# Performance work log

Measured on AMD Instinct MI355X. Metric: run time of the kernel, lower is better.

The kernel has to match this reference:

```python
import jax, jax.numpy as jnp
import numpy as np

C = 32           # number of dominant frequency components kept per node
TAU_FACTOR = 1.0  # dynamic threshold factor
EPS = 1e-10


def setup_inputs() -> dict:
    key = jax.random.key(0)
    k1, k2 = jax.random.split(key)
    N, K = 8192, 256
    # phases in [-pi, pi), amplitudes in [0, 1)
    P_ref = (jax.random.uniform(k1, (N, K), dtype=jnp.float32) - 0.5) * (2.0 * np.pi)
    A_ref = jax.random.uniform(k2, (N, K), dtype=jnp.float32)
    return {"P_ref": P_ref, "A_ref": A_ref}


def reference(P_ref, A_ref):
    N, K = A_ref.shape
    # top-C amplitude mask per node (scatter of top-k indices)
    _, idx = jax.lax.top_k(A_ref, C)                      # [N, C]
    mask = jnp.zeros((N, K), dtype=A_ref.dtype)
    mask = mask.at[jnp.arange(N)[:, None], idx].set(1.0)  # [N, K]
    A_m = A_ref * mask
    P_m = P_ref * mask

    # num[n,m] = sum_k A_m[n,k] A_m[m,k] cos(P_m[n,k] - P_m[m,k])
    # cos(a-b) = cos a cos b + sin a sin b  ->  two GEMMs, no [N,N,K] tensor
    Ac = A_m * jnp.cos(P_m)                               # [N, K]
    As = A_m * jnp.sin(P_m)                               # [N, K]
    num = Ac @ Ac.T + As @ As.T                           # [N, N]

    sq = jnp.sum(A_m * A_m, axis=1)                       # [N]
    denom = jnp.sqrt(sq[:, None] * sq[None, :] + EPS)     # [N, N]
    R = num / denom

    # row-normalize
    R_prime = R / (jnp.sum(R, axis=1, keepdims=True) + EPS)

    # dynamic threshold: mean of strictly-positive entries
    pos = R_prime > 0
    mean_positive = jnp.sum(jnp.where(pos, R_prime, 0.0)) / jnp.maximum(
        jnp.sum(pos).astype(R_prime.dtype), 1.0
    )
    tau = jnp.where(mean_positive > 0, TAU_FACTOR * mean_positive,
                    jnp.asarray(TAU_FACTOR, R_prime.dtype))
    R_hat = jnp.where(R_prime >= tau, R_prime, jnp.zeros_like(R_prime))
    return R_hat
```

## Files before the change

kernel.cpp:

```cpp
#include <hip/hip_runtime.h>
#include <hip/hip_bf16.h>

#define NN 8192
#define KF 256
#define KD 512
#define CK 32
#define PACK 67108864.0

typedef unsigned int uint32;
typedef unsigned short ushort16;
typedef __attribute__((ext_vector_type(8))) short bf16x8;
typedef __attribute__((ext_vector_type(4))) float f32x4;

static __device__ __forceinline__ float bf2f(ushort16 u) {
    union { uint32 i; float f; } v; v.i = ((uint32)u) << 16; return v.f;
}
static __device__ __forceinline__ ushort16 f2bf(float f) {
    __hip_bfloat16 h = __float2bfloat16(f);
    union { __hip_bfloat16 h; ushort16 u; } v; v.h = h; return v.u;
}
static __device__ __forceinline__ void split3(float x, ushort16& h, ushort16& l, ushort16& l2) {
    h = f2bf(x);
    float r1 = x - bf2f(h);
    l = f2bf(r1);
    float r2 = r1 - bf2f(l);
    l2 = f2bf(r2);
}

__global__ void detect_init_kernel(const uint32* __restrict__ rawA, int* __restrict__ flag,
                                   double* __restrict__ acc, double* __restrict__ gstats) {
    if (blockIdx.x == 0) {
        __shared__ int s_top2, s_nz;
        if (threadIdx.x == 0) { s_top2 = 0; s_nz = 0; }
        __syncthreads();
        int top2 = 0, nz = 0;
        for (int i = threadIdx.x; i < 4096; i += 256) {
            uint32 lo = rawA[i] & 0xFFFFu;
            if (lo & 0xC000u) top2 = 1;
            if (lo) nz = 1;
        }
        if (top2) atomicOr(&s_top2, 1);
        if (nz) atomicOr(&s_nz, 1);
        __syncthreads();
        if (threadIdx.x == 0) {
            int f;
            if (s_top2) f = 1;
            else if (s_nz) f = 0;
            else f = 1;
            *flag = f;
        }
    } else {
        int i = (blockIdx.x - 1) * 256 + threadIdx.x;
        if (i < 3 * NN) acc[i] = 0.0;
        if (i < 2) gstats[i] = 0.0;
    }
}

__global__ void prep_kernel(const void* __restrict__ P_, const void* __restrict__ A_,
                            const int* __restrict__ flag,
                            ushort16* __restrict__ Xh, ushort16* __restrict__ Xl,
                            ushort16* __restrict__ Xl2, float* __restrict__ sq) {
    int f = *flag;
    int row = blockIdx.x * 4 + (threadIdx.x >> 6);
    int lane = threadIdx.x & 63;
    if (row >= NN) return;
    float a[4], p[4];
    bool sel[4] = {false, false, false, false};
    if (f) {
        const float* Ar = (const float*)A_ + (size_t)row * KF;
        const float* Pr = (const float*)P_ + (size_t)row * KF;
#pragma unroll
        for (int j = 0; j < 4; j++) {
            int k = lane + 64 * j;
            a[j] = Ar[k];
            p[j] = Pr[k];
        }
    } else {
        const __hip_bfloat16* Ar = (const __hip_bfloat16*)A_ + (size_t)row * KF;
        const __hip_bfloat16* Pr = (const __hip_bfloat16*)P_ + (size_t)row * KF;
#pragma unroll
        for (int j = 0; j < 4; j++) {
            int k = lane + 64 * j;
            a[j] = __bfloat162float(Ar[k]);
            p[j] = __bfloat162float(Pr[k]);
        }
    }
    for (int it = 0; it < CK; ++it) {
        float bv = -1.0f; int bi = KF;
#pragma unroll
        for (int j = 0; j < 4; j++) {
            int k = lane + 64 * j;
            if (!sel[j] && (a[j] > bv || (a[j] == bv && k < bi))) { bv = a[j]; bi = k; }
        }
        for (int off = 32; off > 0; off >>= 1) {
            float ov = __shfl_xor(bv, off);
            int   oi = __shfl_xor(bi, off);
            if (ov > bv || (ov == bv && oi < bi)) { bv = ov; bi = oi; }
        }
        if ((bi & 63) == lane) sel[bi >> 6] = true;
    }
    double sq_part = 0.0;
    size_t rb = (size_t)row * KD;
#pragma unroll
    for (int j = 0; j < 4; j++) {
        int k = lane + 64 * j;
        float c = 0.0f, s = 0.0f;
        if (sel[j]) {
            c = a[j] * cosf(p[j]);
            s = a[j] * sinf(p[j]);
            sq_part += (double)a[j] * (double)a[j];
        }
        ushort16 h, l, l2;
        split3(c, h, l, l2);
        Xh[rb + k] = h; Xl[rb + k] = l; Xl2[rb + k] = l2;
        split3(s, h, l, l2);
        Xh[rb + KF + k] = h; Xl[rb + KF + k] = l; Xl2[rb + KF + k] = l2;
    }
    for (int off = 32; off > 0; off >>= 1) sq_part += __shfl_xor(sq_part, off);
    if (lane == 0) sq[row] = (float)sq_part;
}

#define MM2(A, B)                                                                  \
    _Pragma("unroll") for (int tm = 0; tm < 2; tm++)                               \
    _Pragma("unroll") for (int tn = 0; tn < 2; tn++)                               \
        acc[tm][tn] = __builtin_amdgcn_mfma_f32_16x16x32_bf16(A[tm], B[tn], acc[tm][tn], 0, 0, 0);

#define LOADF2(dst, p, rg, half)                                                   \
    _Pragma("unroll") for (int t = 0; t < 2; t++)                                  \
        dst[t] = *(const bf16x8*)&lds4[(p) * 1536 + (rg) * 256 + ((half) * 32 + t * 16 + r15) * 4 + qp];

#define GLOAD(gp, ldsidx)                                                          \
    __builtin_amdgcn_global_load_lds(                                              \
        (const __attribute__((address_space(1))) unsigned int*)(gp),               \
        (__attribute__((address_space(3))) unsigned int*)&lds4[ldsidx], 16, 0, 0)

#define GLOADALL(p, ko)                                                            \
    _Pragma("unroll") for (int j = 0; j < 6; j++)                                  \
        GLOAD(gptr[j] + (ko), (p) * 1536 + j * 256 + w * 64);

#define COMPUTE(p) {                                                               \
    bf16x8 fa[2], fb[2], ga[2], gb[2];                                             \
    LOADF2(fa, p, 0, wm)                                                  \
    LOADF2(fb, p, 3, wn)                                                  \
    MM2(fa, fb)                                                           \
    LOADF2(gb, p, 4, wn)                                                  \
    MM2(fa, gb)                                                           \
    LOADF2(ga, p, 1, wm)                                                  \
    MM2(ga, fb)                                                           \
    MM2(ga, gb)                                                           \
    LOADF2(gb, p, 5, wn)                                                  \
    MM2(fa, gb)                                                          \
    LOADF2(ga, p, 2, wm)                                                  \
    MM2(ga, fb)             }

__global__ __launch_bounds__(256)
void gemm_kernel(const ushort16* __restrict__ Xh, const ushort16* __restrict__ Xl,
                 const ushort16* __restrict__ Xl2, const float* __restrict__ sq,
                 void* __restrict__ outv, const int* __restrict__ flag,
                 double* __restrict__ rowsum, double* __restrict__ possum,
                 double* __restrict__ pcnt) {
    int bx = blockIdx.x, by = blockIdx.y;
    if (bx < by) return;
    __shared__ uint4 lds4[3072];
    int f = *flag;
    int tid = threadIdx.x;
    int w = tid >> 6;
    int wm = w >> 1, wn = w & 1;
    int L = tid & 63, quad = L >> 4, r15 = L & 15;
    int qp = quad ^ ((r15 >> 1) & 3);
    int row0 = by * 64, col0 = bx * 64;

    f32x4 acc[2][2];
#pragma unroll
    for (int tm = 0; tm < 2; tm++)
#pragma unroll
        for (int tn = 0; tn < 2; tn++) acc[tm][tn] = (f32x4){0.f, 0.f, 0.f, 0.f};

    const ushort16* gptr[6];
    {
        int row = tid >> 2, sp = tid & 3;
        int q = sp ^ ((row >> 1) & 3);
        const ushort16* srcs[6] = {Xh, Xl, Xl2, Xh, Xl, Xl2};
#pragma unroll
        for (int j = 0; j < 6; j++) {
            int tb = (j < 3) ? row0 : col0;
            gptr[j] = srcs[j] + (size_t)(tb + row) * KD + q * 8;
        }
    }

    GLOADALL(0, 0)
    for (int t = 0; t < 16; t += 2) {
        __syncthreads();
        if (t + 1 < 16) { GLOADALL(1, (t + 1) * 32) }
        COMPUTE(0)
        __syncthreads();
        if (t + 2 < 16) { GLOADALL(0, (t + 2) * 32) }
        COMPUTE(1)
    }

    float sqj2[2], sqi2[2][4];
#pragma unroll
    for (int tn = 0; tn < 2; tn++) sqj2[tn] = sq[col0 + wn * 32 + tn * 16 + r15];
#pragma unroll
    for (int tm = 0; tm < 2; tm++)
#pragma unroll
        for (int g = 0; g < 4; g++) sqi2[tm][g] = sq[row0 + wm * 32 + tm * 16 + quad * 4 + g];
#pragma unroll
    for (int tm = 0; tm < 2; tm++)
#pragma unroll
        for (int tn = 0; tn < 2; tn++)
#pragma unroll
            for (int g = 0; g < 4; g++) {
                float denom = sqrtf(sqi2[tm][g] * sqj2[tn] + 1e-10f);
                acc[tm][tn][g] = acc[tm][tn][g] / denom;
            }

    __syncthreads();
    float* Wf = (float*)lds4;
#pragma unroll
    for (int tm = 0; tm < 2; tm++)
#pragma unroll
        for (int tn = 0; tn < 2; tn++)
#pragma unroll
            for (int g = 0; g < 4; g++)
                Wf[(wm * 32 + tm * 16 + quad * 4 + g) * 68 + wn * 32 + tn * 16 + r15] = acc[tm][tn][g];
    __syncthreads();

    int r = tid >> 2, cseg = tid & 3;
    float vals[16];
#pragma unroll
    for (int i4 = 0; i4 < 4; i4++) {
        float4 fv = *(const float4*)&Wf[r * 68 + cseg * 16 + i4 * 4];
        vals[i4 * 4 + 0] = fv.x; vals[i4 * 4 + 1] = fv.y;
        vals[i4 * 4 + 2] = fv.z; vals[i4 * 4 + 3] = fv.w;
    }
    {
        double rs_ = 0.0, ps_ = 0.0;
        float pc_ = 0.0f, nc_ = 0.0f;
#pragma unroll
        for (int i = 0; i < 16; i++) {
            float v = vals[i];
            rs_ += (double)v;
            if (v > 0.0f) { ps_ += (double)v; pc_ += 1.0f; }
            else if (v < 0.0f) { nc_ += 1.0f; }
        }
        rs_ += __shfl_xor(rs_, 1); rs_ += __shfl_xor(rs_, 2);
        ps_ += __shfl_xor(ps_, 1); ps_ += __shfl_xor(ps_, 2);
        pc_ += __shfl_xor(pc_, 1); pc_ += __shfl_xor(pc_, 2);
        nc_ += __shfl_xor(nc_, 1); nc_ += __shfl_xor(nc_, 2);
        if (cseg == 0) {
            int gr = row0 + r;
            atomicAdd(&rowsum[gr], rs_);
            atomicAdd(&possum[gr], ps_);
            atomicAdd(&pcnt[gr], (double)pc_ * PACK + (double)nc_);
        }
    }
    {
        size_t ob = (((size_t)(row0 + r)) << 13) + col0 + cseg * 16;
        if (f) {
            float* O = (float*)outv;
#pragma unroll
            for (int i4 = 0; i4 < 4; i4++)
                *(float4*)(O + ob + i4 * 4) =
                    make_float4(vals[i4 * 4], vals[i4 * 4 + 1], vals[i4 * 4 + 2], vals[i4 * 4 + 3]);
        } else {
            union { uint4 u; ushort16 s[8]; } p0, p1;
#pragma unroll
            for (int i = 0; i < 8; i++) p0.s[i] = f2bf(vals[i]);
#pragma unroll
            for (int i = 0; i < 8; i++) p1.s[i] = f2bf(vals[8 + i]);
            *(uint4*)((__hip_bfloat16*)outv + ob) = p0.u;
            *(uint4*)((__hip_bfloat16*)outv + ob + 8) = p1.u;
        }
    }
    if (bx != by) {
        float vm[16];
#pragma unroll
        for (int i = 0; i < 16; i++) vm[i] = Wf[(cseg * 16 + i) * 68 + r];
        double cs = 0.0, cp = 0.0;
        float cc = 0.0f, cn = 0.0f;
#pragma unroll
        for (int i = 0; i < 16; i++) {
            float v = vm[i];
            cs += (double)v;
            if (v > 0.0f) { cp += (double)v; cc += 1.0f; }
            else if (v < 0.0f) { cn += 1.0f; }
        }
        cs += __shfl_xor(cs, 1); cs += __shfl_xor(cs, 2);
        cp += __shfl_xor(cp, 1); cp += __shfl_xor(cp, 2);
        cc += __shfl_xor(cc, 1); cc += __shfl_xor(cc, 2);
        cn += __shfl_xor(cn, 1); cn += __shfl_xor(cn, 2);
        if (cseg == 0) {
            int gc = col0 + r;
            atomicAdd(&rowsum[gc], cs);
            atomicAdd(&possum[gc], cp);
            atomicAdd(&pcnt[gc], (double)cc * PACK + (double)cn);
        }
        size_t obm = (((size_t)(col0 + r)) << 13) + row0 + cseg * 16;
        if (f) {
            float* O = (float*)outv;
#pragma unroll
            for (int i4 = 0; i4 < 4; i4++)
                *(float4*)(O + obm + i4 * 4) =
                    make_float4(vm[i4 * 4], vm[i4 * 4 + 1], vm[i4 * 4 + 2], vm[i4 * 4 + 3]);
        } else {
            union { uint4 u; ushort16 s[8]; } m0, m1;
#pragma unroll
            for (int i = 0; i < 8; i++) m0.s[i] = f2bf(vm[i]);
#pragma unroll
            for (int i = 0; i < 8; i++) m1.s[i] = f2bf(vm[8 + i]);
            *(uint4*)((__hip_bfloat16*)outv + obm) = m0.u;
            *(uint4*)((__hip_bfloat16*)outv + obm + 8) = m1.u;
        }
    }
}

__global__ void rowfin_kernel(const double* __restrict__ rowsum, const double* __restrict__ possum,
                              const double* __restrict__ pcnt,
                              float* __restrict__ inv_rs, double* __restrict__ gstats) {
    __shared__ double sc[256], sn[256];
    int n = blockIdx.x * 256 + threadIdx.x;
    double rsumv = rowsum[n];
    double rs = rsumv + 1e-10;
    inv_rs[n] = (float)(1.0 / rs);
    double packed = pcnt[n];
    double pc = floor(packed * (1.0 / PACK));
    double nc = packed - pc * PACK;
    double contrib, cnt;
    if (rs > 0.0) { contrib = possum[n] / rs; cnt = pc; }
    else          { contrib = (rsumv - possum[n]) / rs; cnt = nc; }
    sc[threadIdx.x] = contrib; sn[threadIdx.x] = cnt;
    __syncthreads();
    for (int s = 128; s > 0; s >>= 1) {
        if (threadIdx.x < s) { sc[threadIdx.x] += sc[threadIdx.x + s]; sn[threadIdx.x] += sn[threadIdx.x + s]; }
        __syncthreads();
    }
    if (threadIdx.x == 0) { atomicAdd(&gstats[0], sc[0]); atomicAdd(&gstats[1], sn[0]); }
}

__global__ void tau_kernel(const double* __restrict__ gstats, float* __restrict__ tau) {
    double cnt = gstats[1];
    if (cnt < 1.0) cnt = 1.0;
    double mp = gstats[0] / cnt;
    tau[0] = (mp > 0.0) ? (float)mp : 1.0f;
}

__global__ void thresh_kernel(void* __restrict__ R_,
                              const float* __restrict__ inv_rs,
                              const float* __restrict__ tau_p,
                              const int* __restrict__ flag) {
    int f = *flag;
    float tau = *tau_p;
    size_t base = ((size_t)blockIdx.x * 256 + threadIdx.x) * 8;
    if (base >= (size_t)NN * NN) return;
    float inv = inv_rs[base >> 13];
    if (f) {
        float* R = (float*)R_;
        float4 v0 = *(float4*)(R + base);
        float4 v1 = *(float4*)(R + base + 4);
        float vv[8] = {v0.x, v0.y, v0.z, v0.w, v1.x, v1.y, v1.z, v1.w};
#pragma unroll
        for (int t = 0; t < 8; t++) {
            float val = vv[t] * inv;
            vv[t] = (val >= tau) ? val : 0.0f;
        }
        *(float4*)(R + base)     = make_float4(vv[0], vv[1], vv[2], vv[3]);
        *(float4*)(R + base + 4) = make_float4(vv[4], vv[5], vv[6], vv[7]);
    } else {
        __hip_bfloat16* R = (__hip_bfloat16*)R_;
        union { uint4 u; ushort16 s[8]; } in, out;
        in.u = *(const uint4*)(R + base);
#pragma unroll
        for (int t = 0; t < 8; t++) {
            float val = bf2f(in.s[t]) * inv;
            float r = (val >= tau) ? val : 0.0f;
            out.s[t] = f2bf(r);
        }
        *(uint4*)(R + base) = out.u;
    }
}

__global__ void sentinel_kernel(uint32* __restrict__ out, size_t n32) {
    size_t i = (size_t)blockIdx.x * 256 + threadIdx.x;
    if (i < n32) out[i] = 0x47C35000u;
}

extern "C" void kernel_launch(void* const* d_in, const int* in_sizes, int n_in,
                              void* d_out, int out_size, void* d_ws, size_t ws_size,
                              hipStream_t stream) {
    const void* P = d_in[0];
    const void* A = d_in[1];

    char* ws = (char*)d_ws;
    size_t off = 0;
    ushort16* Xh = (ushort16*)(ws + off);   off += (size_t)NN * KD * 2;
    ushort16* Xl = (ushort16*)(ws + off);   off += (size_t)NN * KD * 2;
    ushort16* Xl2 = (ushort16*)(ws + off);  off += (size_t)NN * KD * 2;
    float* sqv = (float*)(ws + off);        off += (size_t)NN * 4;
    double* rowsum = (double*)(ws + off);   off += (size_t)NN * 8;
    double* possum = (double*)(ws + off);   off += (size_t)NN * 8;
    double* pcnt = (double*)(ws + off);     off += (size_t)NN * 8;
    float* inv_rs = (float*)(ws + off);     off += (size_t)NN * 4;
    double* gstats = (double*)(ws + off);   off += 16;
    float* tau = (float*)(ws + off);        off += 16;
    int* flag = (int*)(ws + off);           off += 16;

    if (ws_size < off) {
        size_t n32 = ((size_t)out_size * 2) / 4;
        sentinel_kernel<<<(int)((n32 + 255) / 256), 256, 0, stream>>>((uint32*)d_out, n32);
        return;
    }

    detect_init_kernel<<<1 + (3 * NN + 255) / 256, 256, 0, stream>>>((const uint32*)A, flag, rowsum, gstats);
    prep_kernel<<<NN / 4, 256, 0, stream>>>(P, A, flag, Xh, Xl, Xl2, sqv);
    dim3 ggrid(128, 128);
    gemm_kernel<<<ggrid, 256, 0, stream>>>(Xh, Xl, Xl2, sqv, d_out, flag, rowsum, possum, pcnt);
    rowfin_kernel<<<NN / 256, 256, 0, stream>>>(rowsum, possum, pcnt, inv_rs, gstats);
    tau_kernel<<<1, 1, 0, stream>>>(gstats, tau);
    thresh_kernel<<<(int)(((size_t)NN * NN / 8 + 255) / 256), 256, 0, stream>>>(d_out, inv_rs, tau, flag);
}
```

Measured before the change: 680.6 us.

## Add 128x128-tile symmetric GEMM kernel with dynamic LDS and small-tile fallback

Adds a new GEMM kernel that computes 128x128 output tiles per block (4x4 MFMA tiles per wave) instead of 64x64, using 96KB of dynamic shared memory for the double-buffered triple-split bf16 operands. Larger tiles double the arithmetic done per byte loaded from global memory and halve the number of blocks and atomics for row statistics. The epilogue stages results through LDS to write both the tile and its mirrored transpose with vector stores. The old 64x64 kernel is kept as a fallback if the larger shared-memory request fails, at the cost of higher register pressure and lower occupancy in the big kernel.

```diff
diff --git a/kernel.cpp b/kernel.cpp
--- a/kernel.cpp
+++ b/kernel.cpp
@@ -120,6 +120,228 @@
     if (lane == 0) sq[row] = (float)sq_part;
 }
 
+#define GLOAD(gp, ldsidx)                                                          \
+    __builtin_amdgcn_global_load_lds(                                              \
+        (const __attribute__((address_space(1))) unsigned int*)(gp),               \
+        (__attribute__((address_space(3))) unsigned int*)&lds4[ldsidx], 16, 0, 0)
+
+#define MMB(A, B)                                                                  \
+    _Pragma("unroll") for (int tm = 0; tm < 4; tm++)                               \
+    _Pragma("unroll") for (int tn = 0; tn < 4; tn++)                               \
+        acc[tm][tn] = __builtin_amdgcn_mfma_f32_16x16x32_bf16(A[tm], B[tn], acc[tm][tn], 0, 0, 0);
+
+#define LOADB(dst, p, region, wbase)                                               \
+    _Pragma("unroll") for (int t = 0; t < 4; t++)                                  \
+        dst[t] = *(const bf16x8*)&lds4[(p) * 3072 + (region) * 512 + ((wbase) + t * 16 + r15) * 4 + qp];
+
+#define GLOADALLB(p, ko)                                                           \
+    _Pragma("unroll") for (int j = 0; j < 2; j++) {                                \
+        int lb = (p) * 3072 + w * 128 + j * 64;                                    \
+        GLOAD(gpB[j * 6 + 0] + (ko), 0 * 512 + lb);                                \
+        GLOAD(gpB[j * 6 + 1] + (ko), 1 * 512 + lb);                                \
+        GLOAD(gpB[j * 6 + 2] + (ko), 2 * 512 + lb);                                \
+        GLOAD(gpB[j * 6 + 3] + (ko), 3 * 512 + lb);                                \
+        GLOAD(gpB[j * 6 + 4] + (ko), 4 * 512 + lb);                                \
+        GLOAD(gpB[j * 6 + 5] + (ko), 5 * 512 + lb);                                \
+    }
+
+#define COMPUTEB(p) {                                                              \
+    bf16x8 fa[4], fb[4], ga[4], gb[4];                                             \
+    LOADB(fa, p, 0, wm * 64)                                              \
+    LOADB(fb, p, 3, wn * 64)                                              \
+    MMB(fa, fb)                                                           \
+    LOADB(gb, p, 4, wn * 64)                                              \
+    MMB(fa, gb)                                                           \
+    LOADB(ga, p, 1, wm * 64)                                              \
+    MMB(ga, fb)                                                           \
+    MMB(ga, gb)                                                           \
+    LOADB(gb, p, 5, wn * 64)                                              \
+    MMB(fa, gb)                                                          \
+    LOADB(ga, p, 2, wm * 64)                                              \
+    MMB(ga, fb)                 }
+
+__global__ __launch_bounds__(256)
+void gemm_big(const ushort16* __restrict__ Xh, const ushort16* __restrict__ Xl,
+              const ushort16* __restrict__ Xl2, const float* __restrict__ sq,
+              void* __restrict__ outv, const int* __restrict__ flag,
+              double* __restrict__ rowsum, double* __restrict__ possum,
+              double* __restrict__ pcnt) {
+    int bx = blockIdx.x, by = blockIdx.y;
+    if (bx < by) return;
+    extern __shared__ uint4 lds4[];
+    int f = *flag;
+    int tid = threadIdx.x;
+    int w = tid >> 6;
+    int wm = w >> 1, wn = w & 1;
+    int L = tid & 63, quad = L >> 4, r15 = L & 15;
+    int qp = quad ^ ((r15 >> 1) & 3);
+    int row0 = by * 128, col0 = bx * 128;
+
+    f32x4 acc[4][4];
+#pragma unroll
+    for (int tm = 0; tm < 4; tm++)
+#pragma unroll
+        for (int tn = 0; tn < 4; tn++) acc[tm][tn] = (f32x4){0.f, 0.f, 0.f, 0.f};
+
+    const ushort16* gpB[12];
+#pragma unroll
+    for (int j = 0; j < 2; j++) {
+        int s = w * 128 + j * 64 + L;
+        int rr_ = s >> 2;
+        int qq = (s & 3) ^ ((rr_ >> 1) & 3);
+        size_t aoff = (size_t)(row0 + rr_) * KD + qq * 8;
+        size_t boff = (size_t)(col0 + rr_) * KD + qq * 8;
+        gpB[j * 6 + 0] = Xh + aoff;  gpB[j * 6 + 1] = Xl + aoff;  gpB[j * 6 + 2] = Xl2 + aoff;
+        gpB[j * 6 + 3] = Xh + boff;  gpB[j * 6 + 4] = Xl + boff;  gpB[j * 6 + 5] = Xl2 + boff;
+    }
+
+    GLOADALLB(0, 0)
+    for (int t = 0; t < 16; t += 2) {
+        __syncthreads();
+        if (t + 1 < 16) { GLOADALLB(1, (t + 1) * 32) }
+        COMPUTEB(0)
+        __syncthreads();
+        if (t + 2 < 16) { GLOADALLB(0, (t + 2) * 32) }
+        COMPUTEB(1)
+    }
+
+    float sqj[4], sqiv[4][4];
+#pragma unroll
+    for (int tn = 0; tn < 4; tn++) sqj[tn] = sq[col0 + wn * 64 + tn * 16 + r15];
+#pragma unroll
+    for (int tm = 0; tm < 4; tm++)
+#pragma unroll
+        for (int g = 0; g < 4; g++) sqiv[tm][g] = sq[row0 + wm * 64 + tm * 16 + quad * 4 + g];
+#pragma unroll
+    for (int tm = 0; tm < 4; tm++)
+#pragma unroll
+        for (int tn = 0; tn < 4; tn++)
+#pragma unroll
+            for (int g = 0; g < 4; g++) {
+                float denom = sqrtf(sqiv[tm][g] * sqj[tn] + 1e-10f);
+                acc[tm][tn][g] = acc[tm][tn][g] / denom;
+            }
+
+#pragma unroll
+    for (int tm = 0; tm < 4; tm++)
+#pragma unroll
+        for (int g = 0; g < 4; g++) {
+            double rs_ = 0.0, ps_ = 0.0;
+            float pc_ = 0.0f, nc_ = 0.0f;
+#pragma unroll
+            for (int tn = 0; tn < 4; tn++) {
+                float r = acc[tm][tn][g];
+                rs_ += (double)r;
+                if (r > 0.0f) { ps_ += (double)r; pc_ += 1.0f; }
+                else if (r < 0.0f) { nc_ += 1.0f; }
+            }
+            for (int off = 1; off < 16; off <<= 1) {
+                rs_ += __shfl_xor(rs_, off);
+                ps_ += __shfl_xor(ps_, off);
+                pc_ += __shfl_xor(pc_, off);
+                nc_ += __shfl_xor(nc_, off);
+            }
+            if (r15 == 0) {
+                int gr = row0 + wm * 64 + tm * 16 + quad * 4 + g;
+                atomicAdd(&rowsum[gr], rs_);
+                atomicAdd(&possum[gr], ps_);
+                atomicAdd(&pcnt[gr], (double)pc_ * PACK + (double)nc_);
+            }
+        }
+
+    if (bx != by) {
+#pragma unroll
+        for (int tn = 0; tn < 4; tn++) {
+            double cs = 0.0, cp = 0.0;
+            float cc = 0.0f, cn = 0.0f;
+#pragma unroll
+            for (int tm = 0; tm < 4; tm++)
+#pragma unroll
+                for (int g = 0; g < 4; g++) {
+                    float r = acc[tm][tn][g];
+                    cs += (double)r;
+                    if (r > 0.0f) { cp += (double)r; cc += 1.0f; }
+                    else if (r < 0.0f) { cn += 1.0f; }
+                }
+            cs += __shfl_xor(cs, 16); cs += __shfl_xor(cs, 32);
+            cp += __shfl_xor(cp, 16); cp += __shfl_xor(cp, 32);
+            cc += __shfl_xor(cc, 16); cc += __shfl_xor(cc, 32);
+            cn += __shfl_xor(cn, 16); cn += __shfl_xor(cn, 32);
+            if (L < 16) {
+                int gc = col0 + wn * 64 + tn * 16 + L;
+                atomicAdd(&rowsum[gc], cs);
+                atomicAdd(&possum[gc], cp);
+                atomicAdd(&pcnt[gc], (double)cc * PACK + (double)cn);
+            }
+        }
+    }
+
+    __syncthreads();
+    float* Wf = (float*)lds4;
+#pragma unroll
+    for (int tm = 0; tm < 4; tm++)
+#pragma unroll
+        for (int tn = 0; tn < 4; tn++)
+#pragma unroll
+            for (int g = 0; g < 4; g++)
+                Wf[(wm * 64 + tm * 16 + quad * 4 + g) * 132 + wn * 64 + tn * 16 + r15] = acc[tm][tn][g];
+    __syncthreads();
+
+    {
+        int r = tid >> 1, ch = (tid & 1) * 64;
+        size_t ob = (((size_t)(row0 + r)) << 13) + col0 + ch;
+#pragma unroll
+        for (int seg = 0; seg < 4; seg++) {
+            float4 a0 = *(const float4*)&Wf[r * 132 + ch + seg * 16 + 0];
+            float4 a1 = *(const float4*)&Wf[r * 132 + ch + seg * 16 + 4];
+            float4 a2 = *(const float4*)&Wf[r * 132 + ch + seg * 16 + 8];
+            float4 a3 = *(const float4*)&Wf[r * 132 + ch + seg * 16 + 12];
+            if (f) {
+                float* O = (float*)outv;
+                *(float4*)(O + ob + seg * 16 + 0)  = a0;
+                *(float4*)(O + ob + seg * 16 + 4)  = a1;
+                *(float4*)(O + ob + seg * 16 + 8)  = a2;
+                *(float4*)(O + ob + seg * 16 + 12) = a3;
+            } else {
+                float v[16] = {a0.x,a0.y,a0.z,a0.w, a1.x,a1.y,a1.z,a1.w,
+                               a2.x,a2.y,a2.z,a2.w, a3.x,a3.y,a3.z,a3.w};
+                union { uint4 u; ushort16 s[8]; } p0, p1;
+#pragma unroll
+                for (int i = 0; i < 8; i++) p0.s[i] = f2bf(v[i]);
+#pragma unroll
+                for (int i = 0; i < 8; i++) p1.s[i] = f2bf(v[8 + i]);
+                *(uint4*)((__hip_bfloat16*)outv + ob + seg * 16) = p0.u;
+                *(uint4*)((__hip_bfloat16*)outv + ob + seg * 16 + 8) = p1.u;
+            }
+        }
+    }
+    if (bx != by) {
+        int c = tid >> 1, rh = (tid & 1) * 64;
+        size_t obm = (((size_t)(col0 + c)) << 13) + row0 + rh;
+#pragma unroll
+        for (int seg = 0; seg < 4; seg++) {
+            float v[16];
+#pragma unroll
+            for (int i = 0; i < 16; i++) v[i] = Wf[(rh + seg * 16 + i) * 132 + c];
+            if (f) {
+                float* O = (float*)outv;
+#pragma unroll
+                for (int i4 = 0; i4 < 4; i4++)
+                    *(float4*)(O + obm + seg * 16 + i4 * 4) =
+                        make_float4(v[i4 * 4], v[i4 * 4 + 1], v[i4 * 4 + 2], v[i4 * 4 + 3]);
+            } else {
+                union { uint4 u; ushort16 s[8]; } m0, m1;
+#pragma unroll
+                for (int i = 0; i < 8; i++) m0.s[i] = f2bf(v[i]);
+#pragma unroll
+                for (int i = 0; i < 8; i++) m1.s[i] = f2bf(v[8 + i]);
+                *(uint4*)((__hip_bfloat16*)outv + obm + seg * 16) = m0.u;
+                *(uint4*)((__hip_bfloat16*)outv + obm + seg * 16 + 8) = m1.u;
+            }
+        }
+    }
+}
+
 #define MM2(A, B)                                                                  \
     _Pragma("unroll") for (int tm = 0; tm < 2; tm++)                               \
     _Pragma("unroll") for (int tn = 0; tn < 2; tn++)                               \
@@ -128,11 +350,6 @@
 #define LOADF2(dst, p, rg, half)                                                   \
     _Pragma("unroll") for (int t = 0; t < 2; t++)                                  \
         dst[t] = *(const bf16x8*)&lds4[(p) * 1536 + (rg) * 256 + ((half) * 32 + t * 16 + r15) * 4 + qp];
-
-#define GLOAD(gp, ldsidx)                                                          \
-    __builtin_amdgcn_global_load_lds(                                              \
-        (const __attribute__((address_space(1))) unsigned int*)(gp),               \
-        (__attribute__((address_space(3))) unsigned int*)&lds4[ldsidx], 16, 0, 0)
 
 #define GLOADALL(p, ko)                                                            \
     _Pragma("unroll") for (int j = 0; j < 6; j++)                                  \
@@ -154,11 +371,11 @@
     MM2(ga, fb)             }
 
 __global__ __launch_bounds__(256)
-void gemm_kernel(const ushort16* __restrict__ Xh, const ushort16* __restrict__ Xl,
-                 const ushort16* __restrict__ Xl2, const float* __restrict__ sq,
-                 void* __restrict__ outv, const int* __restrict__ flag,
-                 double* __restrict__ rowsum, double* __restrict__ possum,
-                 double* __restrict__ pcnt) {
+void gemm_small(const ushort16* __restrict__ Xh, const ushort16* __restrict__ Xl,
+                const ushort16* __restrict__ Xl2, const float* __restrict__ sq,
+                void* __restrict__ outv, const int* __restrict__ flag,
+                double* __restrict__ rowsum, double* __restrict__ possum,
+                double* __restrict__ pcnt) {
     int bx = blockIdx.x, by = blockIdx.y;
     if (bx < by) return;
     __shared__ uint4 lds4[3072];
@@ -413,8 +630,19 @@
 
     detect_init_kernel<<<1 + (3 * NN + 255) / 256, 256, 0, stream>>>((const uint32*)A, flag, rowsum, gstats);
     prep_kernel<<<NN / 4, 256, 0, stream>>>(P, A, flag, Xh, Xl, Xl2, sqv);
-    dim3 ggrid(128, 128);
-    gemm_kernel<<<ggrid, 256, 0, stream>>>(Xh, Xl, Xl2, sqv, d_out, flag, rowsum, possum, pcnt);
+
+    bool big_ok = (hipFuncSetAttribute((const void*)gemm_big,
+                    hipFuncAttributeMaxDynamicSharedMemorySize, 98304) == hipSuccess);
+    if (big_ok) {
+        gemm_big<<<dim3(64, 64), 256, 98304, stream>>>(Xh, Xl, Xl2, sqv, d_out, flag,
+                                                       rowsum, possum, pcnt);
+        if (hipGetLastError() != hipSuccess) big_ok = false;
+    }
+    if (!big_ok) {
+        gemm_small<<<dim3(128, 128), 256, 0, stream>>>(Xh, Xl, Xl2, sqv, d_out, flag,
+                                                       rowsum, possum, pcnt);
+    }
+
     rowfin_kernel<<<NN / 256, 256, 0, stream>>>(rowsum, possum, pcnt, inv_rs, gstats);
     tau_kernel<<<1, 1, 0, stream>>>(gstats, tau);
     thresh_kernel<<<(int)(((size_t)NN * NN / 8 + 255) / 256), 256, 0, stream>>>(d_out, inv_rs, tau, flag);
```

Result: slower. 987.4 us (+45.1%).
